# Kernel tuning notes

Measured on AMD Instinct MI355X. Metric: run time of the kernel, lower is better.

## Reference

```python
import jax, jax.numpy as jnp
import numpy as np

N, F, H, K_SUB, DEPTH = 500_000, 64, 32, 16, 4
N_NODES = 2 ** DEPTH - 1   # 15 internal nodes
N_LEAVES = 2 ** DEPTH      # 16 leaves
SLOPE = 0.01               # torch LeakyReLU default negative_slope


def _leaky(v):
    return jnp.where(v >= 0, v, SLOPE * v)


def setup_inputs() -> dict:
    key = jax.random.key(0)
    ks = jax.random.split(key, 8)
    x = jax.random.normal(ks[0], (N, F), dtype=jnp.float32)
    subset_idx = jax.random.randint(ks[1], (N_NODES, K_SUB), 0, F, dtype=jnp.int32)
    W1 = jax.random.normal(ks[2], (N_NODES, H, K_SUB), dtype=jnp.float32) * (1.0 / np.sqrt(K_SUB))
    b1 = jnp.zeros((N_NODES, H), jnp.float32)
    W2 = jax.random.normal(ks[3], (N_NODES, H, H), dtype=jnp.float32) * (1.0 / np.sqrt(H))
    b2 = jnp.zeros((N_NODES, H), jnp.float32)
    W3 = jax.random.normal(ks[4], (N_NODES, 2, H), dtype=jnp.float32) * (1.0 / np.sqrt(H))
    b3 = jnp.zeros((N_NODES, 2), jnp.float32)
    # leaf 'best' constants (class modes precomputed by populate_best)
    leaf_best = jax.random.randint(ks[5], (N_LEAVES,), 0, 10).astype(jnp.float32)
    return {"x": x, "W1": W1, "b1": b1, "W2": W2, "b2": b2, "W3": W3, "b3": b3,
            "leaf_best": leaf_best, "subset_idx": subset_idx}


def _forward(x, W1, b1, W2, b2, W3, b3, leaf_best, subset_idx):
    n = x.shape[0]
    loc = jnp.zeros((n,), jnp.int32)   # local node index within current level
    off = 0
    for level in range(DEPTH):
        k = 2 ** level
        sl = slice(off, off + k)
        xs = x[:, subset_idx[sl]]                                   # [N, k, K_SUB]
        h = _leaky(jnp.einsum('nkf,khf->nkh', xs, W1[sl]) + b1[sl])  # [N, k, H]
        h = _leaky(jnp.einsum('nkh,kgh->nkg', h, W2[sl]) + b2[sl])   # [N, k, H]
        logits = jnp.einsum('nkh,koh->nko', h, W3[sl]) + b3[sl]      # [N, k, 2]
        p0 = jax.nn.softmax(logits, axis=-1)[..., 0]                 # [N, k]
        p0_row = jnp.take_along_axis(p0, loc[:, None], axis=1)[:, 0]
        bit = (p0_row < 0.5).astype(jnp.int32)  # 0 -> left, 1 -> right
        loc = 2 * loc + bit
        off += k
    return leaf_best[loc]  # [N]


def reference(x, W1, b1, W2, b2, W3, b3, leaf_best, subset_idx):
    return _forward(x, W1, b1, W2, b2, W3, b3, leaf_best, subset_idx)
```

## Files before the change

kernel.cpp:

```cpp
#include <hip/hip_runtime.h>

#define NF 64
#define NH 32
#define NK 16
#define NNODES 15
#define BLOCK 512
#define NWAVES (BLOCK / 64)


__global__ __attribute__((amdgpu_flat_work_group_size(512, 512),
                          amdgpu_waves_per_eu(2, 4)))
void tree_mlp_kernel(
    const float* __restrict__ x,
    const float* __restrict__ W1, const float* __restrict__ b1,
    const float* __restrict__ W2, const float* __restrict__ b2,
    const float* __restrict__ W3, const float* __restrict__ b3,
    const float* __restrict__ leaf_best, const int* __restrict__ subset_idx,
    float* __restrict__ out, int N)
{
    __shared__ __align__(16) float W2L[NNODES * 1024];
    __shared__ int      subL[NNODES * NK];
    __shared__ unsigned permL[BLOCK];
    __shared__ int      sortL[NWAVES * 16];

    const int tid  = threadIdx.x;
    const int lane = tid & 63;
    const int wv   = tid >> 6;

    for (int i = tid; i < NNODES * 1024; i += BLOCK) W2L[i] = W2[i];
    for (int i = tid; i < NNODES * NK;   i += BLOCK) subL[i] = subset_idx[i];
    __syncthreads();

    const int s = blockIdx.x * BLOCK + tid;
    int valid = (s < N) ? 1 : 0;
    int id    = valid ? s : 0;
    int loc = 0, off = 0;

    #pragma unroll 1
    for (int level = 0; level < 4; ++level) {
        if (level > 0) {
            const int nb = 1 << level;
            int myrank = 0;
            #pragma unroll 1
            for (int b = 0; b < nb; ++b) {
                const unsigned long long m = __ballot(loc == b);
                if (loc == b)
                    myrank = __popcll(m & ((1ull << lane) - 1ull));
                if (lane == 0)
                    sortL[b * NWAVES + wv] = __popcll(m);
            }
            __syncthreads();
            if (tid == 0) {
                int run = 0;
                for (int i = 0; i < nb * NWAVES; ++i) {
                    const int c = sortL[i];
                    sortL[i] = run;
                    run += c;
                }
            }
            __syncthreads();
            const int slot = sortL[loc * NWAVES + wv] + myrank;
            permL[slot] = ((unsigned)id << 5) | ((unsigned)valid << 4) | (unsigned)loc;
            __syncthreads();
            const unsigned p = permL[tid];
            id    = (int)(p >> 5);
            valid = (int)((p >> 4) & 1u);
            loc   = (int)(p & 15u);
            __syncthreads();
        }

        const int node = off + loc;
        const float* xr = x + (size_t)id * NF;

        float xs[NK];
        const int* si = subL + node * NK;
        #pragma unroll
        for (int k = 0; k < NK; ++k) xs[k] = xr[si[k]];

        float h1v[NH];
        const float4* w1g = (const float4*)(W1 + node * (NH * NK));
        const float* b1g = b1 + node * NH;
        #pragma unroll
        for (int j = 0; j < NH; ++j) {
            float acc = b1g[j];
            #pragma unroll
            for (int q = 0; q < NK / 4; ++q) {
                const float4 t = w1g[j * 4 + q];
                acc += t.x * xs[q * 4 + 0];
                acc += t.y * xs[q * 4 + 1];
                acc += t.z * xs[q * 4 + 2];
                acc += t.w * xs[q * 4 + 3];
            }
            h1v[j] = (acc >= 0.f) ? acc : 0.01f * acc;
        }

        float h2v[NH];
        const float4* w2n = (const float4*)(W2L + node * 1024);
        const float* b2g = b2 + node * NH;
        #pragma unroll
        for (int g = 0; g < NH; ++g) {
            float acc = b2g[g];
            #pragma unroll
            for (int q = 0; q < NH / 4; ++q) {
                const float4 t = w2n[g * 8 + q];
                acc += t.x * h1v[q * 4 + 0];
                acc += t.y * h1v[q * 4 + 1];
                acc += t.z * h1v[q * 4 + 2];
                acc += t.w * h1v[q * 4 + 3];
            }
            h2v[g] = (acc >= 0.f) ? acc : 0.01f * acc;
        }

        const float4* w3g = (const float4*)(W3 + node * 2 * NH);
        float l0 = b3[node * 2 + 0];
        float l1 = b3[node * 2 + 1];
        #pragma unroll
        for (int q = 0; q < NH / 4; ++q) {
            const float4 t0 = w3g[q];
            l0 += t0.x * h2v[q * 4 + 0];
            l0 += t0.y * h2v[q * 4 + 1];
            l0 += t0.z * h2v[q * 4 + 2];
            l0 += t0.w * h2v[q * 4 + 3];
        }
        #pragma unroll
        for (int q = 0; q < NH / 4; ++q) {
            const float4 t1 = w3g[8 + q];
            l1 += t1.x * h2v[q * 4 + 0];
            l1 += t1.y * h2v[q * 4 + 1];
            l1 += t1.z * h2v[q * 4 + 2];
            l1 += t1.w * h2v[q * 4 + 3];
        }

        const int bit = (l0 < l1) ? 1 : 0;
        loc = 2 * loc + bit;
        off = 2 * off + 1;
    }

    if (valid) out[id] = leaf_best[loc];
}

extern "C" void kernel_launch(void* const* d_in, const int* in_sizes, int n_in,
                              void* d_out, int out_size, void* d_ws, size_t ws_size,
                              hipStream_t stream) {
    const float* x         = (const float*)d_in[0];
    const float* W1        = (const float*)d_in[1];
    const float* b1        = (const float*)d_in[2];
    const float* W2        = (const float*)d_in[3];
    const float* b2        = (const float*)d_in[4];
    const float* W3        = (const float*)d_in[5];
    const float* b3        = (const float*)d_in[6];
    const float* leaf_best = (const float*)d_in[7];
    const int*   subset    = (const int*)d_in[8];

    const int N = in_sizes[0] / NF;
    const int grid = (N + BLOCK - 1) / BLOCK;
    tree_mlp_kernel<<<grid, BLOCK, 0, stream>>>(
        x, W1, b1, W2, b2, W3, b3, leaf_best, subset, (float*)d_out, N);
}
```

Before: 497.0 us.

## Read wave-uniform node weights as scalar loads and drop W2 LDS staging

Removes the per-block copy of all W2 weights into LDS. Each wave now loops over the node range it spans and, for each node present, evaluates the MLP with wave-uniform weight addresses so loads can become scalar. The block size grows to 640 threads with a waves-per-EU hint of 5, and the sort scratch is shrunk. The trade-off is redundant MLP work for waves that straddle several nodes, plus higher register pressure from the larger block.

```diff
diff --git a/kernel.cpp b/kernel.cpp
--- a/kernel.cpp
+++ b/kernel.cpp
@@ -4,12 +4,12 @@
 #define NH 32
 #define NK 16
 #define NNODES 15
-#define BLOCK 512
+#define BLOCK 640
 #define NWAVES (BLOCK / 64)
 
 
-__global__ __attribute__((amdgpu_flat_work_group_size(512, 512),
-                          amdgpu_waves_per_eu(2, 4)))
+__global__ __attribute__((amdgpu_flat_work_group_size(BLOCK, BLOCK),
+                          amdgpu_waves_per_eu(5)))
 void tree_mlp_kernel(
     const float* __restrict__ x,
     const float* __restrict__ W1, const float* __restrict__ b1,
@@ -18,17 +18,15 @@
     const float* __restrict__ leaf_best, const int* __restrict__ subset_idx,
     float* __restrict__ out, int N)
 {
-    __shared__ __align__(16) float W2L[NNODES * 1024];
     __shared__ int      subL[NNODES * NK];
     __shared__ unsigned permL[BLOCK];
-    __shared__ int      sortL[NWAVES * 16];
+    __shared__ int      sortL[NWAVES * 8];
 
     const int tid  = threadIdx.x;
     const int lane = tid & 63;
     const int wv   = tid >> 6;
 
-    for (int i = tid; i < NNODES * 1024; i += BLOCK) W2L[i] = W2[i];
-    for (int i = tid; i < NNODES * NK;   i += BLOCK) subL[i] = subset_idx[i];
+    for (int i = tid; i < NNODES * NK; i += BLOCK) subL[i] = subset_idx[i];
     __syncthreads();
 
     const int s = blockIdx.x * BLOCK + tid;
@@ -77,61 +75,49 @@
         #pragma unroll
         for (int k = 0; k < NK; ++k) xs[k] = xr[si[k]];
 
-        float h1v[NH];
-        const float4* w1g = (const float4*)(W1 + node * (NH * NK));
-        const float* b1g = b1 + node * NH;
-        #pragma unroll
-        for (int j = 0; j < NH; ++j) {
-            float acc = b1g[j];
+        int bit = 0;
+        const int nd0 = __builtin_amdgcn_readfirstlane(node);
+        const int nd1 = __builtin_amdgcn_readlane(node, 63);
+
+        #pragma unroll 1
+        for (int nd = nd0; nd <= nd1; ++nd) {
+            if (!__any(node == nd)) continue;
+
+            const float* w1  = W1 + nd * (NH * NK);
+            const float* bb1 = b1 + nd * NH;
+            const float* w2  = W2 + nd * (NH * NH);
+            const float* bb2 = b2 + nd * NH;
+            const float* w3  = W3 + nd * (2 * NH);
+            const float* bb3 = b3 + nd * 2;
+
+            float h1v[NH];
             #pragma unroll
-            for (int q = 0; q < NK / 4; ++q) {
-                const float4 t = w1g[j * 4 + q];
-                acc += t.x * xs[q * 4 + 0];
-                acc += t.y * xs[q * 4 + 1];
-                acc += t.z * xs[q * 4 + 2];
-                acc += t.w * xs[q * 4 + 3];
+            for (int j = 0; j < NH; ++j) {
+                float acc = bb1[j];
+                #pragma unroll
+                for (int k = 0; k < NK; ++k) acc += w1[j * NK + k] * xs[k];
+                h1v[j] = (acc >= 0.f) ? acc : 0.01f * acc;
             }
-            h1v[j] = (acc >= 0.f) ? acc : 0.01f * acc;
+
+            float h2v[NH];
+            #pragma unroll
+            for (int g = 0; g < NH; ++g) {
+                float acc = bb2[g];
+                #pragma unroll
+                for (int k = 0; k < NH; ++k) acc += w2[g * NH + k] * h1v[k];
+                h2v[g] = (acc >= 0.f) ? acc : 0.01f * acc;
+            }
+
+            float l0 = bb3[0];
+            float l1 = bb3[1];
+            #pragma unroll
+            for (int k = 0; k < NH; ++k) l0 += w3[k] * h2v[k];
+            #pragma unroll
+            for (int k = 0; k < NH; ++k) l1 += w3[NH + k] * h2v[k];
+
+            if (node == nd) bit = (l0 < l1) ? 1 : 0;
         }
 
-        float h2v[NH];
-        const float4* w2n = (const float4*)(W2L + node * 1024);
-        const float* b2g = b2 + node * NH;
-        #pragma unroll
-        for (int g = 0; g < NH; ++g) {
-            float acc = b2g[g];
-            #pragma unroll
-            for (int q = 0; q < NH / 4; ++q) {
-                const float4 t = w2n[g * 8 + q];
-                acc += t.x * h1v[q * 4 + 0];
-                acc += t.y * h1v[q * 4 + 1];
-                acc += t.z * h1v[q * 4 + 2];
-                acc += t.w * h1v[q * 4 + 3];
-            }
-            h2v[g] = (acc >= 0.f) ? acc : 0.01f * acc;
-        }
-
-        const float4* w3g = (const float4*)(W3 + node * 2 * NH);
-        float l0 = b3[node * 2 + 0];
-        float l1 = b3[node * 2 + 1];
-        #pragma unroll
-        for (int q = 0; q < NH / 4; ++q) {
-            const float4 t0 = w3g[q];
-            l0 += t0.x * h2v[q * 4 + 0];
-            l0 += t0.y * h2v[q * 4 + 1];
-            l0 += t0.z * h2v[q * 4 + 2];
-            l0 += t0.w * h2v[q * 4 + 3];
-        }
-        #pragma unroll
-        for (int q = 0; q < NH / 4; ++q) {
-            const float4 t1 = w3g[8 + q];
-            l1 += t1.x * h2v[q * 4 + 0];
-            l1 += t1.y * h2v[q * 4 + 1];
-            l1 += t1.z * h2v[q * 4 + 2];
-            l1 += t1.w * h2v[q * 4 + 3];
-        }
-
-        const int bit = (l0 < l1) ? 1 : 0;
         loc = 2 * loc + bit;
         off = 2 * off + 1;
     }
```

Result: slower. 870.5 us (+75.1%).
